# Optimization experiments

Measured on AMD Instinct MI355X. Metric: run time of the kernel, lower is better.

## Reference

```python
import jax, jax.numpy as jnp
import numpy as np

N = 1026; DX = 4096; DG = 4096; H0 = 4096; H1 = 2048; H2 = 1024
OUTS = 512; NL = 10; JH = 2048; E = 32832; K = 128; ALPHA = 0.05
INS = DX + DG  # 8192, edgeconv1 / joint_gemb input width

def _w(k, fan_in, shape):
    s = 1.0 / np.sqrt(fan_in)
    return jax.random.uniform(k, shape, minval=-s, maxval=s, dtype=jnp.float32)

def setup_inputs() -> dict:
    key = jax.random.key(0)
    ks = jax.random.split(key, 32)
    return dict(
        x=jax.random.normal(ks[0], (N, DX), jnp.float32),
        gx=jax.random.normal(ks[1], (N, DG), jnp.float32),
        edge_index=jax.random.randint(ks[2], (2, E), 0, N, dtype=jnp.int32),
        jw1=_w(ks[3], INS, (INS, JH)), jb1=_w(ks[4], INS, (JH,)),
        jw2=_w(ks[5], JH, (JH, N)), jb2=_w(ks[6], JH, (N,)),
        ec1_w=_w(ks[7], INS, (INS, H0)), ec1_b=_w(ks[8], INS, (H0,)),
        dr_w=_w(ks[9], H0, (H0, H2)), dr_b=_w(ks[10], H0, (H2,)),
        g1_w=_w(ks[11], H0, (H0, H1)), g1_b=_w(ks[12], H0, (H1,)),
        g2_w=_w(ks[13], H1, (H1, H2)), g2_b=_w(ks[14], H1, (H2,)),
        ec2_w=_w(ks[15], H2 + H1 + H0, (H2 + H1 + H0, H2)), ec2_b=_w(ks[16], H2 + H1 + H0, (H2,)),
        ec3_w=_w(ks[17], H2, (H2, OUTS)), ec3_b=_w(ks[18], H2, (OUTS,)),
        out_w=_w(ks[19], OUTS, (OUTS, NL)), out_b=_w(ks[20], OUTS, (NL,)),
    )

def _gdc(A):
    # GDC: self_loop_weight=1, sym norm in, exact PPR (alpha), topk(k, dim=0) sparsify, col norm out
    n = A.shape[0]
    eye = jnp.eye(n, dtype=A.dtype)
    A = A + eye  # self loops, weight 1
    deg = A.sum(axis=1)
    dinv = jax.lax.rsqrt(jnp.where(deg > 0, deg, 1.0))
    T = dinv[:, None] * A * dinv[None, :]          # D^-1/2 (A+I) D^-1/2
    S = ALPHA * jnp.linalg.inv(eye - (1.0 - ALPHA) * T)  # exact PPR diffusion
    vals, idx = jax.lax.top_k(S.T, K)              # top-K per column (dim=0)
    St = jnp.zeros((n, n), S.dtype).at[jnp.arange(n)[:, None], idx].set(vals)
    S = St.T
    csum = S.sum(axis=0)
    return S / jnp.where(csum == 0, 1.0, csum)[None, :]  # col normalization out

def _gcn(h_in, W, b, row, col, n):
    # PyG GCNConv: add self loops, sym-normalized aggregation, then bias
    h = h_in @ W
    deg = jax.ops.segment_sum(jnp.ones(row.shape[0], h.dtype), col, num_segments=n) + 1.0
    dinv = jax.lax.rsqrt(deg)
    agg = jax.ops.segment_sum(h[row] * (dinv[row] * dinv[col])[:, None], col, num_segments=n)
    return agg + h * (dinv * dinv)[:, None] + b

def _forward(x, gx, edge_index, jw1, jb1, jw2, jb2, ec1_w, ec1_b, dr_w, dr_b,
             g1_w, g1_b, g2_w, g2_b, ec2_w, ec2_b, ec3_w, ec3_b, out_w, out_b):
    row, col = edge_index[0], edge_index[1]
    xg = jnp.concatenate([x, gx], axis=1)                    # [N, INS]
    zz = jax.nn.relu(jax.nn.relu(xg @ jw1 + jb1) @ jw2 + jb2)  # joint_gemb -> [N, N] adjacency
    zz = _gdc(zz)
    xn = zz @ x                                              # nconv: dense neighbor aggregation
    z = jax.nn.relu(jnp.concatenate([xn, gx], axis=1) @ ec1_w + ec1_b)  # [N, H0]
    z0 = z @ dr_w + dr_b                                     # [N, H2]
    z1 = jax.nn.relu(_gcn(z + gx, g1_w, g1_b, row, col, N))  # [N, H1]
    z2 = jax.nn.relu(_gcn(z1, g2_w, g2_b, row, col, N))      # [N, H2]
    zc = jax.nn.relu(jnp.concatenate([z, z1, z2], axis=1) @ ec2_w + ec2_b)
    zf = jax.nn.relu((zc + z0) @ ec3_w + ec3_b)
    return zf @ out_w + out_b                                # [N, NL]

def reference(x, gx, edge_index, jw1, jb1, jw2, jb2, ec1_w, ec1_b, dr_w, dr_b,
              g1_w, g1_b, g2_w, g2_b, ec2_w, ec2_b, ec3_w, ec3_b, out_w, out_b):
    return _forward(x, gx, edge_index, jw1, jb1, jw2, jb2, ec1_w, ec1_b, dr_w, dr_b,
                    g1_w, g1_b, g2_w, g2_b, ec2_w, ec2_b, ec3_w, ec3_b, out_w, out_b)
```

## Files before the change

### kernel.cpp

```cpp
#include <hip/hip_runtime.h>
#include <stdint.h>

static constexpr int N_   = 1026;
static constexpr int DX_  = 4096;
static constexpr int DG_  = 4096;
static constexpr int H0_  = 4096;
static constexpr int H1_  = 2048;
static constexpr int H2_  = 1024;
static constexpr int OUTS_= 512;
static constexpr int NL_  = 10;
static constexpr int JH_  = 2048;
static constexpr int E_   = 32832;
static constexpr int K_   = 128;
static constexpr int INS_ = DX_ + DG_;
static constexpr int CAT2_= H0_ + H1_ + H2_;

static constexpr int MP_   = 1152;
static constexpr int KP1_  = 1056;

typedef _Float16 f16;
typedef __attribute__((ext_vector_type(8))) _Float16 f16x8;
typedef __attribute__((ext_vector_type(4))) _Float16 f16x4;
typedef __attribute__((ext_vector_type(4))) float    f32x4;

#define AS1C(p) ((const __attribute__((address_space(1))) unsigned int*)(p))
#define AS3(p)  ((__attribute__((address_space(3))) unsigned int*)(p))

__device__ __forceinline__ void gload16(const f16* g, f16* s) {
    __builtin_amdgcn_global_load_lds(AS1C(g), AS3(s), 16, 0, 0);
}

__device__ __forceinline__ void swz_tile(int gx, int gy, int& bx, int& by) {
    int nwg = gx * gy;
    int hid = blockIdx.x + gx * blockIdx.y;
    int xcd = hid & 7, seq = hid >> 3;
    int q = nwg >> 3, r = nwg & 7;
    int lin = (xcd < r ? xcd * (q + 1) : r * (q + 1) + (xcd - r) * q) + seq;
    bx = lin / gy;  by = lin - bx * gy;
}

template<bool RELU, bool DUAL, bool WIDE>
__global__ __launch_bounds__(512, (DUAL || WIDE) ? 4 : 8)
void gemm_f16x2(int M, int Nc, int Kt, int chunkSteps,
                const f16* __restrict__ Ah, const f16* __restrict__ Al, int lda,
                const f16* __restrict__ Bh, const f16* __restrict__ Bl, int ldb,
                const float* __restrict__ bias, float alpha,
                const float* __restrict__ D, int ldd, float dscale,
                float* __restrict__ C, int ldc,
                f16* __restrict__ oAh, f16* __restrict__ oAl, int ldoa,
                f16* __restrict__ oBh, f16* __restrict__ oBl, int ldob,
                float* __restrict__ P, int Mp, int Ncp)
// ... 157 lines not shown
        if (oAl) oAl[(size_t)row * ldoa + col] = (f16)(val - (float)h);
    }
    if (oBh) {
        f16 h = (f16)val;
        oBh[(size_t)col * ldob + row] = h;
        if (oBl) oBl[(size_t)col * ldob + row] = (f16)(val - (float)h);
    }
}

__global__ __launch_bounds__(512, 4)
void pchain_k(int roleBase, int split, int chunkSteps,
              const f16* __restrict__ uAh, const f16* __restrict__ uAl,
              const f16* __restrict__ sAh, const f16* __restrict__ sAl,
              const f16* __restrict__ Bh, const f16* __restrict__ Bl,
              float* __restrict__ Pp)
{
    __shared__ __align__(16) f16 sm[2][4][4096];
    const int tid  = threadIdx.x;
    const int lane = tid & 63, w = tid >> 6;
    const int wr = w >> 1, wc = w & 1;
    int bx, by; swz_tile(gridDim.x, gridDim.y, bx, by);
    const int bm = by * 128, bn = bx * 128;
    const int z = blockIdx.z;
    const int role = roleBase + z / split;
    const int sub  = z % split;
    const f16* Ah = (role == 0) ? uAh : sAh;
    const f16* Al = (role == 0) ? uAl : sAl;

    const int sBeg = sub * chunkSteps;
    int nst = KP1_ / 32 - sBeg; if (nst > chunkSteps) nst = chunkSteps;

    const int srow  = w * 16 + (tid & 15);
    const int skoff = ((tid >> 4) & 3) * 8;
    const size_t arow = (size_t)(bm + srow) * KP1_ + skoff;
    const size_t brow = (size_t)(bn + srow) * KP1_ + skoff;
    const int wslot = w * 512;
    const int fr = (lane >> 4) * 128 + (lane & 15) * 8;
    const int iaBase = wr * 1024 + fr;
    const int ibBase = wc * 2048 + fr;

    f32x4 acc[2][4] = {};

    auto stage = [&](int buf, size_t ka) {
        f16* s0 = (f16*)&sm[buf][0][0];
        gload16(Ah + arow + ka, s0 + wslot);
        gload16(Al + arow + ka, s0 + 4096 + wslot);
        gload16(Bh + brow + ka, s0 + 8192 + wslot);
        gload16(Bl + brow + ka, s0 + 12288 + wslot);
    };

    if (nst > 0) {
        const size_t kb = (size_t)sBeg * 32;
        stage(0, kb);
        for (int s = 0; s < nst; ++s) {
            if (s + 1 < nst) {
                stage((s + 1) & 1, kb + (size_t)(s + 1) * 32);
                asm volatile("s_waitcnt vmcnt(4)\n\ts_barrier" ::: "memory");
            } else {
                asm volatile("s_waitcnt vmcnt(0)\n\ts_barrier" ::: "memory");
            }
            const int b = s & 1;
            f16x8 ah[2], al[2], bh4[4], bl4[4];
            #pragma unroll
            for (int i = 0; i < 2; ++i) {
                ah[i]  = *(const f16x8*)&sm[b][0][iaBase + i * 512];
                al[i]  = *(const f16x8*)&sm[b][1][iaBase + i * 512];
            }
            #pragma unroll
// ... 21 lines not shown
    for (int mi = 0; mi < 2; ++mi)
        #pragma unroll
        for (int nj = 0; nj < 4; ++nj) {
            const int gc = n00 + nj * 16 + ec;
            const int gr = m00 + mi * 16 + er;
            float* p = Pz + (size_t)gr * 1152 + gc;
            f32x4 a = acc[mi][nj];
            #pragma unroll
            for (int r = 0; r < 4; ++r) p[(size_t)r * 1152] = a[r];
        }
}

__global__ __launch_bounds__(256)
void pchain_combine_k(int nz, int hasUpd, int hasSq, const float* __restrict__ Pp,
                      const float* __restrict__ PfIn, float* __restrict__ PfOut,
                      f16* __restrict__ oPh, f16* __restrict__ oPl,
                      float* __restrict__ XT,
                      f16* __restrict__ oAh, f16* __restrict__ oAl,
                      f16* __restrict__ oAth, f16* __restrict__ oAtl)
{
    unsigned idx = blockIdx.x * 256 + threadIdx.x;
    if (idx >= (unsigned)(N_ * N_)) return;
    int row = idx / (unsigned)N_, col = idx - row * N_;
    const size_t zs = (size_t)1152 * 1152;
    const size_t poff = (size_t)row * 1152 + col;
    int zb = 0;
    if (hasUpd) {
        float s = 0.f;
        for (int z = 0; z < nz; ++z) s += Pp[(size_t)(zb + z) * zs + poff];
        float val = s + PfIn[idx];
        PfOut[idx] = val;
        if (oPh) {
            f16 h = (f16)val, l = (f16)(val - (float)h);
            oPh[(size_t)row * KP1_ + col] = h;
            oPl[(size_t)row * KP1_ + col] = l;
        }
        if (XT) XT[(size_t)col * N_ + row] = val;
        zb += nz;
    }
    if (hasSq) {
        float s = 0.f;
        for (int z = 0; z < nz; ++z) s += Pp[(size_t)(zb + z) * zs + poff];
        f16 h = (f16)s, l = (f16)(s - (float)h);
        oAh[(size_t)row * KP1_ + col] = h;  oAl[(size_t)row * KP1_ + col] = l;
        oAth[(size_t)col * KP1_ + row] = h; oAtl[(size_t)col * KP1_ + row] = l;
    }
}

__global__ void build_A_k(const float* __restrict__ zz, const float* __restrict__ dinv,
                          f16* __restrict__ aAh, f16* __restrict__ aAl,
                          f16* __restrict__ aBth, f16* __restrict__ aBtl,
                          float* __restrict__ Pf,
                          f16* __restrict__ pAh, f16* __restrict__ pAl)
{
    int idx = blockIdx.x * 256 + threadIdx.x;
    if (idx >= N_ * N_) return;
    int i = idx / N_, j = idx - i * N_;
    float diag = (i == j) ? 1.f : 0.f;
    float a = 0.95f * dinv[i] * (zz[idx] + diag) * dinv[j];
    f16 h = (f16)a, l = (f16)(a - (float)h);
    aAh[(size_t)i * KP1_ + j] = h;  aAl[(size_t)i * KP1_ + j] = l;
    aBth[(size_t)j * KP1_ + i] = h; aBtl[(size_t)j * KP1_ + i] = l;
    float p = a + diag;
    Pf[idx] = p;
    f16 ph = (f16)p, pl = (f16)(p - (float)ph);
    pAh[(size_t)i * KP1_ + j] = ph; pAl[(size_t)i * KP1_ + j] = pl;
}

__global__ __launch_bounds__(256)
void topk_sort_k(const float* __restrict__ XT, float* __restrict__ S)
{
    __shared__ uint64_t key[2048];
    __shared__ float red[4];
    const int j = blockIdx.x, t = threadIdx.x;
    for (int i = t; i < 2048; i += 256) {
        uint64_t kk;
        if (i < N_) {
            float v = XT[(size_t)j * N_ + i];
            unsigned u = __float_as_uint(v);
            unsigned sv = (u & 0x80000000u) ? ~u : (u | 0x80000000u);
            kk = ((uint64_t)(~sv) << 32) | (unsigned)i;
        } else kk = ~0ULL;
        key[i] = kk;
    }
    __syncthreads();
    for (int k = 2; k <= 2048; k <<= 1) {
        for (int jj = k >> 1; jj > 0; jj >>= 1) {
            #pragma unroll
            for (int q = 0; q < 8; ++q) {
                int i = t + q * 256;
                int ixj = i ^ jj;
                if (ixj > i) {
                    uint64_t a = key[i], b = key[ixj];
                    bool up = ((i & k) == 0);
                    if ((a > b) == up) { key[i] = b; key[ixj] = a; }
                }
            }
            __syncthreads();
        }
    }
    float val = 0.f; int idx = 0;
    if (t < K_) {
        uint64_t kk = key[t];
        unsigned sv = ~(unsigned)(kk >> 32);
        unsigned u = (sv & 0x80000000u) ? (sv & 0x7FFFFFFFu) : ~sv;
        val = __uint_as_float(u);
        idx = (int)(kk & 0xFFFFFFFFu);
    }
    float sm = (t < K_) ? val : 0.f;
    #pragma unroll
    for (int q = 32; q > 0; q >>= 1) sm += __shfl_xor(sm, q);
    if ((t & 63) == 0) red[t >> 6] = sm;
    __syncthreads();
    float cs = red[0] + red[1] + red[2] + red[3];
    if (cs == 0.f) cs = 1.f;
    if (t < K_) S[(size_t)idx * N_ + j] = val / cs;
}

__global__ void conv_A_k(const float* __restrict__ src, int R, int C, int lds,
                         f16* __restrict__ dh, f16* __restrict__ dl, int ldd,
                         int Rp, int Cp)
{
    size_t i4 = ((size_t)blockIdx.x * 256 + threadIdx.x) * 4;
    if (i4 >= (size_t)Rp * Cp) return;
    int r = (int)(i4 / Cp), c = (int)(i4 % Cp);
    float v[4] = {0.f, 0.f, 0.f, 0.f};
    if (r < R) {
        if (((lds & 3) == 0) && c + 3 < C) {
            float4 f = *(const float4*)&src[(size_t)r * lds + c];
            v[0] = f.x; v[1] = f.y; v[2] = f.z; v[3] = f.w;
        } else {
            #pragma unroll
            for (int q = 0; q < 4; ++q) v[q] = (c + q < C) ? src[(size_t)r * lds + c + q] : 0.f;
        }
    }
    f16x4 h, l;
    #pragma unroll
    for (int q = 0; q < 4; ++q) { h[q] = (f16)v[q]; l[q] = (f16)(v[q] - (float)h[q]); }
    *(f16x4*)&dh[(size_t)r * ldd + c] = h;
    if (dl) *(f16x4*)&dl[(size_t)r * ldd + c] = l;
}

__global__ __launch_bounds__(256)
void conv_Bt_k(const float* __restrict__ src, int K, int N,
               f16* __restrict__ dh, f16* __restrict__ dl, int ldk,
               int Kp, int Np)
{
// ... 28 lines not shown
        #pragma unroll
        for (int p = 0; p < 2; ++p) {
            int n = bn + nn0 + p * 32;
            int k = bk + k4;
            if (n < Np && k < Kp) {
                f16x4 h, l;
                #pragma unroll
                for (int q = 0; q < 4; ++q) {
                    float vv = t[k4 + q][nn0 + p * 32];
                    h[q] = (f16)vv; l[q] = (f16)(vv - (float)h[q]);
                }
                *(f16x4*)&dh[(size_t)n * ldk + k] = h;
                if (dl) *(f16x4*)&dl[(size_t)n * ldk + k] = l;
            }
        }
    }
}

__global__ void cat2_conv_k(const float* __restrict__ a, const float* __restrict__ b,
                            f16* __restrict__ dh, f16* __restrict__ dl)
{
    size_t i4 = ((size_t)blockIdx.x * 256 + threadIdx.x) * 4;
    if (i4 >= (size_t)MP_ * 8192) return;
    int r = (int)(i4 / 8192), c = (int)(i4 % 8192);
    float v[4] = {0.f, 0.f, 0.f, 0.f};
    if (r < N_) {
        const float* s = (c < 4096) ? &a[(size_t)r * 4096 + c] : &b[(size_t)r * 4096 + (c - 4096)];
        float4 f = *(const float4*)s;
        v[0] = f.x; v[1] = f.y; v[2] = f.z; v[3] = f.w;
    }
    f16x4 h, l;
    #pragma unroll
    for (int q = 0; q < 4; ++q) { h[q] = (f16)v[q]; l[q] = (f16)(v[q] - (float)h[q]); }
    *(f16x4*)&dh[i4] = h;
    *(f16x4*)&dl[i4] = l;
}

__global__ void zgx_conv_k(const f16* __restrict__ zh, const float* __restrict__ gx,
                           f16* __restrict__ dh)
{
    size_t i4 = ((size_t)blockIdx.x * 256 + threadIdx.x) * 4;
    if (i4 >= (size_t)MP_ * 4096) return;
    int r = (int)(i4 / 4096), c = (int)(i4 % 4096);
    f16x4 h = {};
    if (r < N_) {
        f16x4 zh4 = *(const f16x4*)&zh[(size_t)r * CAT2_ + c];
        float4 g4 = *(const float4*)&gx[(size_t)r * 4096 + c];
        float gv[4] = {g4.x, g4.y, g4.z, g4.w};
        #pragma unroll
        for (int q = 0; q < 4; ++q) h[q] = (f16)((float)zh4[q] + gv[q]);
    }
    *(f16x4*)&dh[i4] = h;
}

__global__ void zc_conv_k(const float* __restrict__ zc, const float* __restrict__ z0,
                          f16* __restrict__ dh)
{
    size_t i4 = ((size_t)blockIdx.x * 256 + threadIdx.x) * 4;
    if (i4 >= (size_t)MP_ * 1024) return;
    int r = (int)(i4 / 1024), c = (int)(i4 % 1024);
    f16x4 h = {};
    if (r < N_) {
        float4 a4 = *(const float4*)&zc[(size_t)r * 1024 + c];
        float4 b4 = *(const float4*)&z0[(size_t)r * 1024 + c];
        float av[4] = {a4.x, a4.y, a4.z, a4.w};
        float bv[4] = {b4.x, b4.y, b4.z, b4.w};
        #pragma unroll
        for (int q = 0; q < 4; ++q) h[q] = (f16)(av[q] + bv[q]);
    }
    *(f16x4*)&dh[i4] = h;
}

template<int NPARTS, bool RELU>
__global__ __launch_bounds__(256)
void gemm_k(int M, int Nc, int Kt,
            const float* __restrict__ A0, int w0,
            const float* __restrict__ A1, int w1,
            const float* __restrict__ A2, int w2,
            const float* __restrict__ B, int ldb,
            const float* __restrict__ bias,
            float alpha, const float* __restrict__ D, float dscale,
            float* __restrict__ C, int ldc)
{
    __shared__ __align__(16) float As[16][68];
    __shared__ __align__(16) float Bs[16][68];
    const int tid = threadIdx.x;
    const int tx = tid & 15, ty = tid >> 4;
    const int bm = blockIdx.y * 64, bn = blockIdx.x * 64;
    const int w01 = w0 + w1;
    float acc[4][4] = {};

    for (int kt = 0; kt < Kt; kt += 16) {
        #pragma unroll
        for (int r = 0; r < 4; ++r) {
            int idx = tid + r * 256;
            int m = idx >> 4, kk = idx & 15;
            int row = bm + m, k = kt + kk;
            float v = 0.f;
            if (row < M && k < Kt) {
                if (NPARTS == 1) v = A0[(size_t)row * w0 + k];
                else {
                    if (k < w0) v = A0[(size_t)row * w0 + k];
                    else if (NPARTS == 2 || k < w01) v = A1[(size_t)row * w1 + (k - w0)];
// ... 194 lines not shown
            combine_k<false><<<cg, 256, 0, st>>>(M, Nc, split, Mp, Ncp, P, bias, alpha,
                D, ldd, dscale, C, ldc, oA.h, oA.l, ldoa, oB.h, oB.l, ldob);
    }
}

static inline void convA(hipStream_t st, const float* src, int R, int C, int lds,
                         HL d, int ldd, int Rp, int Cp)
{
    size_t total4 = (size_t)Rp * Cp / 4;
    conv_A_k<<<(int)((total4 + 255) / 256), 256, 0, st>>>(src, R, C, lds, d.h, d.l, ldd, Rp, Cp);
}
static inline void convBt(hipStream_t st, const float* src, int K, int N,
                          HL d, int ldk, int Kp, int Np)
{
    dim3 grid((Kp + 31) / 32, (Np + 63) / 64), blk(256);
    conv_Bt_k<<<grid, blk, 0, st>>>(src, K, N, d.h, d.l, ldk, Kp, Np);
}

static inline void launch_gemm_f32(hipStream_t st, bool relu, int nparts,
                                   int M, int Nc, int Kt,
                                   const float* A0, int w0, const float* A1, int w1,
                                   const float* A2, int w2,
                                   const float* B, int ldb, const float* bias,
                                   float alpha, const float* D, float dscale,
                                   float* C, int ldc)
{
    dim3 g((Nc + 63) / 64, (M + 63) / 64), b(256);
#define CALL_GEMM(NP, RL) gemm_k<NP, RL><<<g, b, 0, st>>>(M, Nc, Kt, A0, w0, A1, w1, A2, w2, B, ldb, bias, alpha, D, dscale, C, ldc)
    if (relu) { if (nparts == 1) CALL_GEMM(1, true); else if (nparts == 2) CALL_GEMM(2, true); else CALL_GEMM(3, true); }
    else      { if (nparts == 1) CALL_GEMM(1, false); else if (nparts == 2) CALL_GEMM(2, false); else CALL_GEMM(3, false); }
#undef CALL_GEMM
}

static constexpr size_t catA1_e = (size_t)MP_ * 8192;
static constexpr size_t jw1Bt_e = (size_t)2048 * 8192;
static constexpr size_t jw2Bt_e = (size_t)MP_ * 2048;
static constexpr size_t h1A_e   = (size_t)MP_ * 2048;
static constexpr size_t nb_e    = (size_t)MP_ * KP1_;
static constexpr size_t ec1Bt_e = (size_t)4096 * 8192;
static constexpr size_t drBt_e  = (size_t)1024 * 4096;
static constexpr size_t g1Bt_e  = (size_t)2048 * 4096;
static constexpr size_t g2Bt_e  = (size_t)1024 * 2048;
static constexpr size_t ec2Bt_e = (size_t)1024 * 7168;
static constexpr size_t ec3Bt_e = (size_t)512 * 1024;
static constexpr size_t hg1Bt_e = (size_t)2048 * KP1_;
static constexpr size_t hg2Bt_e = (size_t)1024 * KP1_;
static constexpr size_t catA2_e = (size_t)MP_ * 8192;
static constexpr size_t SA_e    = nb_e;
static constexpr size_t GA_e    = nb_e;
static constexpr size_t xBt_e   = (size_t)4096 * KP1_;
static constexpr size_t zgxA_e  = (size_t)MP_ * 4096;
static constexpr size_t cat3_e  = (size_t)MP_ * 7168;
static constexpr size_t zcA_e   = (size_t)MP_ * 1024;

static constexpr size_t u_catA1 = 0;
static constexpr size_t u_jw1Bt = u_catA1 + 2 * catA1_e;
static constexpr size_t u_jw2Bt = u_jw1Bt + 2 * jw1Bt_e;
static constexpr size_t u_h1A   = u_jw2Bt + 2 * jw2Bt_e;
static constexpr size_t u_nb0   = u_h1A + 2 * h1A_e;
static constexpr size_t u_nb1   = u_nb0 + 2 * nb_e;
static constexpr size_t u_nb2   = u_nb1 + 2 * nb_e;
static constexpr size_t u_nb3   = u_nb2 + 2 * nb_e;
static constexpr size_t u_nb4   = u_nb3 + 2 * nb_e;
static constexpr size_t u_nb5   = u_nb4 + 2 * nb_e;
static constexpr size_t UNION_F16 = u_nb5 + 2 * nb_e;
static_assert(2 * ec1Bt_e <= UNION_F16, "ec1Bt alias");
static constexpr size_t u_drBt  = 0;
static constexpr size_t u_g1Bt  = u_drBt + 2 * drBt_e;
static constexpr size_t u_g2Bt  = u_g1Bt + 2 * g1Bt_e;
static constexpr size_t u_ec2Bt = u_g2Bt + 2 * g2Bt_e;
static constexpr size_t u_ec3Bt = u_ec2Bt + 2 * ec2Bt_e;
static constexpr size_t u_hg1Bt = u_ec3Bt + 2 * ec3Bt_e;
static constexpr size_t u_hg2Bt = u_hg1Bt + 2 * hg1Bt_e;
static_assert(u_hg2Bt + 2 * hg2Bt_e <= UNION_F16, "phase3 alias");

static constexpr size_t o_catA2 = 0;
static constexpr size_t o_SA    = o_catA2 + 2 * catA2_e;
static constexpr size_t o_GA    = o_SA + 2 * SA_e;
static constexpr size_t o_xBt   = o_GA + 2 * GA_e;
static constexpr size_t o_zgxA  = o_xBt + 2 * xBt_e;
static constexpr size_t o_cat3  = o_zgxA + 2 * zgxA_e;
static constexpr size_t o_zcA   = o_cat3 + 2 * cat3_e;
static constexpr size_t OUT_F16 = o_zcA + 2 * zcA_e;

static constexpr size_t NN_     = (size_t)N_ * N_;
static constexpr size_t F16_TOTAL = UNION_F16 + OUT_F16;
static constexpr size_t f_zz = 0, f_Mm = NN_, f_X0 = 2 * NN_, f_X1 = 3 * NN_,
                        f_S = 4 * NN_, f_G = 5 * NN_, f_z0 = 6 * NN_,
                        f_zc = f_z0 + (size_t)N_ * 1024,
                        f_zf = f_zc + (size_t)N_ * 1024,
                        f_dinv = f_zf + (size_t)N_ * 512,
                        f_dinv2 = f_dinv + 1028,
                        F32_TOTAL = f_dinv2 + 1028;
static constexpr size_t P_e = (size_t)2 * MP_ * 4096;
static constexpr size_t FAST_WS_BYTES = F16_TOTAL * 2 + (F32_TOTAL + P_e) * 4;
static_assert((size_t)6 * 1152 * 1152 <= P_e, "pchain partial fit");
static_assert((size_t)8 * 1152 * 1024 <= P_e, "wide split8 fit");
static_assert((size_t)4 * 1152 * 2048 <= P_e, "wide split4 fit");

static void run_fast(void* const* d_in, float* out, void* d_ws, hipStream_t st)
{
    const float* x    = (const float*)d_in[0];
    const float* gx   = (const float*)d_in[1];
    const int*   ei   = (const int*)d_in[2];
    const float* jw1  = (const float*)d_in[3];
    const float* jb1  = (const float*)d_in[4];
    const float* jw2  = (const float*)d_in[5];
    const float* jb2  = (const float*)d_in[6];
    const float* ec1w = (const float*)d_in[7];
    const float* ec1b = (const float*)d_in[8];
    const float* drw  = (const float*)d_in[9];
    const float* drb  = (const float*)d_in[10];
    const float* g1w  = (const float*)d_in[11];
    const float* g1b  = (const float*)d_in[12];
    const float* g2w  = (const float*)d_in[13];
    const float* g2b  = (const float*)d_in[14];
    const float* ec2w = (const float*)d_in[15];
    const float* ec2b = (const float*)d_in[16];
    const float* ec3w = (const float*)d_in[17];
    const float* ec3b = (const float*)d_in[18];
    const float* outw = (const float*)d_in[19];
    const float* outb = (const float*)d_in[20];

    f16*   fb   = (f16*)d_ws;
    float* f32b = (float*)((char*)d_ws + F16_TOTAL * 2);
    float* P    = f32b + F32_TOTAL;

    auto mk = [&](size_t off, size_t elems) { return HL{fb + off, fb + off + elems}; };
    HL catA1 = mk(u_catA1, catA1_e), jw1Bt = mk(u_jw1Bt, jw1Bt_e),
       jw2Bt = mk(u_jw2Bt, jw2Bt_e), h1A = mk(u_h1A, h1A_e);
    HL pA[2]  = {mk(u_nb0, nb_e), mk(u_nb1, nb_e)};
    HL aA[2]  = {mk(u_nb2, nb_e), mk(u_nb3, nb_e)};
    HL aBt[2] = {mk(u_nb4, nb_e), mk(u_nb5, nb_e)};
    HL ec1Bt = mk(0, ec1Bt_e);
    HL drBt = mk(u_drBt, drBt_e), g1Bt = mk(u_g1Bt, g1Bt_e), g2Bt = mk(u_g2Bt, g2Bt_e),
       ec2Bt = mk(u_ec2Bt, ec2Bt_e), ec3Bt = mk(u_ec3Bt, ec3Bt_e),
       hg1Bt = mk(u_hg1Bt, hg1Bt_e), hg2Bt = mk(u_hg2Bt, hg2Bt_e);
    HL catA2 = mk(UNION_F16 + o_catA2, catA2_e), SA = mk(UNION_F16 + o_SA, SA_e),
       GA = mk(UNION_F16 + o_GA, GA_e), xBt = mk(UNION_F16 + o_xBt, xBt_e),
       zgxA = mk(UNION_F16 + o_zgxA, zgxA_e), cat3 = mk(UNION_F16 + o_cat3, cat3_e),
       zcA = mk(UNION_F16 + o_zcA, zcA_e);
    float *zz = f32b + f_zz, *XT = f32b + f_Mm, *Pf[2] = {f32b + f_X0, f32b + f_X1},
          *S = f32b + f_S, *G = f32b + f_G, *z0 = f32b + f_z0, *zc = f32b + f_zc,
          *zf = f32b + f_zf, *dinv = f32b + f_dinv, *dinv2 = f32b + f_dinv2;

    hipMemsetAsync(fb + u_nb0, 0, (UNION_F16 - u_nb0) * sizeof(f16), st);

    {
        size_t t4 = (size_t)MP_ * 8192 / 4;
        cat2_conv_k<<<(int)((t4 + 255) / 256), 256, 0, st>>>(x, gx, catA1.h, catA1.l);
    }
    convBt(st, jw1, 8192, 2048, jw1Bt, 8192, 8192, 2048);
    g16(st, true, true, false, 1026, 2048, 8192, 4, catA1, 8192, jw1Bt, 8192, jb1, 1.f,
        nullptr, 0, 0.f, nullptr, 0, h1A, 2048, HL0, 0, P);
    convBt(st, jw2, 2048, 1026, jw2Bt, 2048, 2048, MP_);
    g16(st, true, true, false, 1026, 1026, 2048, 7, h1A, 2048, jw2Bt, 2048, jb2, 1.f,
        nullptr, 0, 0.f, zz, 1026, HL0, 0, HL0, 0, P);
    row_dinv_k<<<N_, 256, 0, st>>>(zz, dinv);
    build_A_k<<<(int)((NN_ + 255) / 256), 256, 0, st>>>(zz, dinv,
        aA[0].h, aA[0].l, aBt[0].h, aBt[0].l, Pf[0], pA[0].h, pA[0].l);
    {
        const int PS = 3, PCH = 11;
        dim3 cg((unsigned)((NN_ + 255) / 256));
        pchain_k<<<dim3(9, 9, PS), 512, 0, st>>>(1, PS, PCH,
            nullptr, nullptr, aA[0].h, aA[0].l, aBt[0].h, aBt[0].l, P);
        pchain_combine_k<<<cg, 256, 0, st>>>(PS, 0, 1, P,
            nullptr, nullptr, nullptr, nullptr, nullptr,
            aA[1].h, aA[1].l, aBt[1].h, aBt[1].l);
        int ac = 1, pc = 0;
        for (int k = 2; k <= 7; ++k) {
            pchain_k<<<dim3(9, 9, 2 * PS), 512, 0, st>>>(0, PS, PCH,
                pA[pc].h, pA[pc].l, aA[ac].h, aA[ac].l, aBt[ac].h, aBt[ac].l, P);
            pchain_combine_k<<<cg, 256, 0, st>>>(PS, 1, 1, P,
                Pf[pc], Pf[1 - pc], pA[1 - pc].h, pA[1 - pc].l, nullptr,
                aA[1 - ac].h, aA[1 - ac].l, aBt[1 - ac].h, aBt[1 - ac].l);
            pc ^= 1; ac ^= 1;
        }
        pchain_k<<<dim3(9, 9, PS), 512, 0, st>>>(0, PS, PCH,
            pA[pc].h, pA[pc].l, nullptr, nullptr, aBt[ac].h, aBt[ac].l, P);
        pchain_combine_k<<<cg, 256, 0, st>>>(PS, 1, 0, P,
            Pf[pc], Pf[1 - pc], nullptr, nullptr, XT,
            nullptr, nullptr, nullptr, nullptr);
    }
    hipMemsetAsync(S, 0, NN_ * sizeof(float), st);
    topk_sort_k<<<N_, 256, 0, st>>>(XT, S);
    convA(st, S, N_, N_, N_, SA, KP1_, MP_, KP1_);
    convBt(st, x, 1026, 4096, xBt, KP1_, KP1_, 4096);
    g16(st, false, true, false, 1026, 4096, KP1_, 2, SA, KP1_, xBt, KP1_, nullptr, 1.f,
        nullptr, 0, 0.f, nullptr, 0, HL{catA2.h, nullptr}, 8192, HL0, 0, P);
    convA(st, gx, N_, 4096, 4096, HL{catA2.h + 4096, nullptr}, 8192, MP_, 4096);
    convBt(st, ec1w, 8192, 4096, HL{ec1Bt.h, nullptr}, 8192, 8192, 4096);
    g16(st, true, false, true, 1026, 4096, 8192, 2, catA2, 8192, ec1Bt, 8192, ec1b, 1.f,
        nullptr, 0, 0.f, nullptr, 0, HL{cat3.h, nullptr}, 7168, HL0, 0, P);
    deg_dinv_k<<<1, 1024, 0, st>>>(ei, dinv2);
    hipMemsetAsync(G, 0, NN_ * sizeof(float), st);
    edge_diag_G_k<<<(E_ + N_ + 255) / 256, 256, 0, st>>>(ei, dinv2, G);
    convA(st, G, N_, N_, N_, HL{GA.h, nullptr}, KP1_, MP_, KP1_);
    convBt(st, drw, 4096, 1024, HL{drBt.h, nullptr}, 4096, 4096, 1024);
    g16(st, false, false, true, 1026, 1024, 4096, 8, HL{cat3.h, nullptr}, 7168,
        drBt, 4096, drb, 1.f, nullptr, 0, 0.f, z0, 1024, HL0, 0, HL0, 0, P);
    {
        size_t t4 = (size_t)MP_ * 4096 / 4;
        zgx_conv_k<<<(int)((t4 + 255) / 256), 256, 0, st>>>(cat3.h, gx, zgxA.h);
    }
    convBt(st, g1w, 4096, 2048, HL{g1Bt.h, nullptr}, 4096, 4096, 2048);
    hipMemsetAsync(fb + u_hg1Bt, 0, (2 * hg1Bt_e + 2 * hg2Bt_e) * sizeof(f16), st);
    g16(st, false, false, false, 2048, 1026, 4096, 4, g1Bt, 4096, zgxA, 4096, nullptr, 1.f,
        nullptr, 0, 0.f, nullptr, 0, HL{hg1Bt.h, nullptr}, KP1_, HL0, 0, P);
    g16(st, true, false, true, 1026, 2048, KP1_, 4, GA, KP1_, hg1Bt, KP1_, g1b, 1.f,
        nullptr, 0, 0.f, nullptr, 0, HL{cat3.h + 4096, nullptr}, 7168, HL0, 0, P);
    convBt(st, g2w, 2048, 1024, HL{g2Bt.h, nullptr}, 2048, 2048, 1024);
    g16(st, false, false, false, 1024, 1026, 2048, 8, g2Bt, 2048,
        HL{cat3.h + 4096, nullptr}, 7168, nullptr, 1.f, nullptr, 0, 0.f,
        nullptr, 0, HL{hg2Bt.h, nullptr}, KP1_, HL0, 0, P);
    g16(st, true, false, true, 1026, 1024, KP1_, 8, GA, KP1_, hg2Bt, KP1_, g2b, 1.f,
        nullptr, 0, 0.f, nullptr, 0, HL{cat3.h + 6144, nullptr}, 7168, HL0, 0, P);
    convBt(st, ec2w, 7168, 1024, HL{ec2Bt.h, nullptr}, 7168, 7168, 1024);
    g16(st, true, false, true, 1026, 1024, 7168, 8, HL{cat3.h, nullptr}, 7168,
        ec2Bt, 7168, ec2b, 1.f, nullptr, 0, 0.f, zc, 1024, HL0, 0, HL0, 0, P);
    {
        size_t t4 = (size_t)MP_ * 1024 / 4;
        zc_conv_k<<<(int)((t4 + 255) / 256), 256, 0, st>>>(zc, z0, zcA.h);
    }
    convBt(st, ec3w, 1024, 512, HL{ec3Bt.h, nullptr}, 1024, 1024, 512);
    g16(st, true, false, false, 1026, 512, 1024, 8, HL{zcA.h, nullptr}, 1024,
        ec3Bt, 1024, ec3b, 1.f, nullptr, 0, 0.f, zf, 512, HL0, 0, HL0, 0, P);
    launch_gemm_f32(st, false, 1, N_, NL_, OUTS_, zf, OUTS_, nullptr, 0, nullptr, 0,
                    outw, NL_, outb, 1.f, nullptr, 0.f, out, NL_);
}

static void run_ref(void* const* d_in, float* out, void* d_ws, hipStream_t stream)
{
    const float* x    = (const float*)d_in[0];
    const float* gx   = (const float*)d_in[1];
    const int*   ei   = (const int*)d_in[2];
    const float* jw1  = (const float*)d_in[3];
    const float* jb1  = (const float*)d_in[4];
    const float* jw2  = (const float*)d_in[5];
    const float* jb2  = (const float*)d_in[6];
    const float* ec1w = (const float*)d_in[7];
    const float* ec1b = (const float*)d_in[8];
    const float* drw  = (const float*)d_in[9];
    const float* drb  = (const float*)d_in[10];
    const float* g1w  = (const float*)d_in[11];
    const float* g1b  = (const float*)d_in[12];
    const float* g2w  = (const float*)d_in[13];
    const float* g2b  = (const float*)d_in[14];
    const float* ec2w = (const float*)d_in[15];
    const float* ec2b = (const float*)d_in[16];
    const float* ec3w = (const float*)d_in[17];
    const float* ec3b = (const float*)d_in[18];
    const float* outw = (const float*)d_in[19];
    const float* outb = (const float*)d_in[20];

    float* ws = (float*)d_ws;
    size_t off = 0;
    float* H1buf = ws + off; off += (size_t)N_ * JH_;
    float* ZZ    = ws + off; off += NN_;
    float* Mm    = ws + off; off += NN_;
// ... 74 lines not shown
```

Measured before the change: 1.478 ms.

## Pad f16 operand leading dimensions by 64 and widen top-k sort blocks

Adds 64 elements of padding to the leading dimension of every f16 GEMM operand buffer (INS, JH, H0, CAT3, H2, NB). The likely aim is to stop power-of-two row strides from landing repeatedly on the same memory channels or cache sets. Buffers that only ever hold a high part now get single-sized allocations, which shrinks the workspace. The top-k bitonic sort now runs with 512 threads per block instead of 256, halving the per-thread work in each phase. All call sites and conversion kernels are updated, so a missed stride would silently corrupt results.

```diff
diff --git a/kernel.cpp b/kernel.cpp
--- a/kernel.cpp
+++ b/kernel.cpp
@@ -17,6 +17,13 @@
 
 static constexpr int MP_   = 1152;
 static constexpr int KP1_  = 1056;
+
+static constexpr int LD_INS  = INS_ + 64;
+static constexpr int LD_JH   = JH_  + 64;
+static constexpr int LD_H0   = H0_  + 64;
+static constexpr int LD_CAT3 = CAT2_+ 64;
+static constexpr int LD_H2   = H2_  + 64;
+static constexpr int LD_NB   = KP1_ + 64;
 
 typedef _Float16 f16;
 typedef __attribute__((ext_vector_type(8))) _Float16 f16x8;
@@ -240,8 +247,8 @@
 
     const int srow  = w * 16 + (tid & 15);
     const int skoff = ((tid >> 4) & 3) * 8;
-    const size_t arow = (size_t)(bm + srow) * KP1_ + skoff;
-    const size_t brow = (size_t)(bn + srow) * KP1_ + skoff;
+    const size_t arow = (size_t)(bm + srow) * LD_NB + skoff;
+    const size_t brow = (size_t)(bn + srow) * LD_NB + skoff;
     const int wslot = w * 512;
     const int fr = (lane >> 4) * 128 + (lane & 15) * 8;
     const int iaBase = wr * 1024 + fr;
@@ -329,8 +336,8 @@
         PfOut[idx] = val;
         if (oPh) {
             f16 h = (f16)val, l = (f16)(val - (float)h);
-            oPh[(size_t)row * KP1_ + col] = h;
-            oPl[(size_t)row * KP1_ + col] = l;
+            oPh[(size_t)row * LD_NB + col] = h;
+            oPl[(size_t)row * LD_NB + col] = l;
         }
         if (XT) XT[(size_t)col * N_ + row] = val;
         zb += nz;
@@ -339,8 +346,8 @@
         float s = 0.f;
         for (int z = 0; z < nz; ++z) s += Pp[(size_t)(zb + z) * zs + poff];
         f16 h = (f16)s, l = (f16)(s - (float)h);
-        oAh[(size_t)row * KP1_ + col] = h;  oAl[(size_t)row * KP1_ + col] = l;
-        oAth[(size_t)col * KP1_ + row] = h; oAtl[(size_t)col * KP1_ + row] = l;
+        oAh[(size_t)row * LD_NB + col] = h;  oAl[(size_t)row * LD_NB + col] = l;
+        oAth[(size_t)col * LD_NB + row] = h; oAtl[(size_t)col * LD_NB + row] = l;
     }
 }
 
@@ -356,21 +363,21 @@
     float diag = (i == j) ? 1.f : 0.f;
     float a = 0.95f * dinv[i] * (zz[idx] + diag) * dinv[j];
     f16 h = (f16)a, l = (f16)(a - (float)h);
-    aAh[(size_t)i * KP1_ + j] = h;  aAl[(size_t)i * KP1_ + j] = l;
-    aBth[(size_t)j * KP1_ + i] = h; aBtl[(size_t)j * KP1_ + i] = l;
+    aAh[(size_t)i * LD_NB + j] = h;  aAl[(size_t)i * LD_NB + j] = l;
+    aBth[(size_t)j * LD_NB + i] = h; aBtl[(size_t)j * LD_NB + i] = l;
     float p = a + diag;
     Pf[idx] = p;
     f16 ph = (f16)p, pl = (f16)(p - (float)ph);
-    pAh[(size_t)i * KP1_ + j] = ph; pAl[(size_t)i * KP1_ + j] = pl;
-}
-
-__global__ __launch_bounds__(256)
+    pAh[(size_t)i * LD_NB + j] = ph; pAl[(size_t)i * LD_NB + j] = pl;
+}
+
+__global__ __launch_bounds__(512)
 void topk_sort_k(const float* __restrict__ XT, float* __restrict__ S)
 {
     __shared__ uint64_t key[2048];
-    __shared__ float red[4];
+    __shared__ float red[8];
     const int j = blockIdx.x, t = threadIdx.x;
-    for (int i = t; i < 2048; i += 256) {
+    for (int i = t; i < 2048; i += 512) {
         uint64_t kk;
         if (i < N_) {
             float v = XT[(size_t)j * N_ + i];
@@ -384,8 +391,8 @@
     for (int k = 2; k <= 2048; k <<= 1) {
         for (int jj = k >> 1; jj > 0; jj >>= 1) {
             #pragma unroll
-            for (int q = 0; q < 8; ++q) {
-                int i = t + q * 256;
+            for (int q = 0; q < 4; ++q) {
+                int i = t + q * 512;
                 int ixj = i ^ jj;
                 if (ixj > i) {
                     uint64_t a = key[i], b = key[ixj];
@@ -409,7 +416,9 @@
     for (int q = 32; q > 0; q >>= 1) sm += __shfl_xor(sm, q);
     if ((t & 63) == 0) red[t >> 6] = sm;
     __syncthreads();
-    float cs = red[0] + red[1] + red[2] + red[3];
+    float cs = 0.f;
+    #pragma unroll
+    for (int q = 0; q < 8; ++q) cs += red[q];
     if (cs == 0.f) cs = 1.f;
     if (t < K_) S[(size_t)idx * N_ + j] = val / cs;
 }
@@ -504,8 +513,8 @@
     f16x4 h, l;
     #pragma unroll
     for (int q = 0; q < 4; ++q) { h[q] = (f16)v[q]; l[q] = (f16)(v[q] - (float)h[q]); }
-    *(f16x4*)&dh[i4] = h;
-    *(f16x4*)&dl[i4] = l;
+    *(f16x4*)&dh[(size_t)r * LD_INS + c] = h;
+    *(f16x4*)&dl[(size_t)r * LD_INS + c] = l;
 }
 
 __global__ void zgx_conv_k(const f16* __restrict__ zh, const float* __restrict__ gx,
@@ -516,13 +525,13 @@
     int r = (int)(i4 / 4096), c = (int)(i4 % 4096);
     f16x4 h = {};
     if (r < N_) {
-        f16x4 zh4 = *(const f16x4*)&zh[(size_t)r * CAT2_ + c];
+        f16x4 zh4 = *(const f16x4*)&zh[(size_t)r * LD_CAT3 + c];
         float4 g4 = *(const float4*)&gx[(size_t)r * 4096 + c];
         float gv[4] = {g4.x, g4.y, g4.z, g4.w};
         #pragma unroll
         for (int q = 0; q < 4; ++q) h[q] = (f16)((float)zh4[q] + gv[q]);
     }
-    *(f16x4*)&dh[i4] = h;
+    *(f16x4*)&dh[(size_t)r * LD_H0 + c] = h;
 }
 
 __global__ void zc_conv_k(const float* __restrict__ zc, const float* __restrict__ z0,
@@ -540,7 +549,7 @@
         #pragma unroll
         for (int q = 0; q < 4; ++q) h[q] = (f16)(av[q] + bv[q]);
     }
-    *(f16x4*)&dh[i4] = h;
+    *(f16x4*)&dh[(size_t)r * LD_H2 + c] = h;
 }
 
 template<int NPARTS, bool RELU>
@@ -801,26 +810,26 @@
 #undef CALL_GEMM
 }
 
-static constexpr size_t catA1_e = (size_t)MP_ * 8192;
-static constexpr size_t jw1Bt_e = (size_t)2048 * 8192;
-static constexpr size_t jw2Bt_e = (size_t)MP_ * 2048;
-static constexpr size_t h1A_e   = (size_t)MP_ * 2048;
-static constexpr size_t nb_e    = (size_t)MP_ * KP1_;
-static constexpr size_t ec1Bt_e = (size_t)4096 * 8192;
-static constexpr size_t drBt_e  = (size_t)1024 * 4096;
-static constexpr size_t g1Bt_e  = (size_t)2048 * 4096;
-static constexpr size_t g2Bt_e  = (size_t)1024 * 2048;
-static constexpr size_t ec2Bt_e = (size_t)1024 * 7168;
-static constexpr size_t ec3Bt_e = (size_t)512 * 1024;
-static constexpr size_t hg1Bt_e = (size_t)2048 * KP1_;
-static constexpr size_t hg2Bt_e = (size_t)1024 * KP1_;
-static constexpr size_t catA2_e = (size_t)MP_ * 8192;
+static constexpr size_t catA1_e = (size_t)MP_ * LD_INS;
+static constexpr size_t jw1Bt_e = (size_t)2048 * LD_INS;
+static constexpr size_t jw2Bt_e = (size_t)MP_ * LD_JH;
+static constexpr size_t h1A_e   = (size_t)MP_ * LD_JH;
+static constexpr size_t nb_e    = (size_t)MP_ * LD_NB;
+static constexpr size_t ec1Bt_e = (size_t)4096 * LD_INS;
+static constexpr size_t drBt_e  = (size_t)1024 * LD_H0;
+static constexpr size_t g1Bt_e  = (size_t)2048 * LD_H0;
+static constexpr size_t g2Bt_e  = (size_t)1024 * LD_JH;
+static constexpr size_t ec2Bt_e = (size_t)1024 * LD_CAT3;
+static constexpr size_t ec3Bt_e = (size_t)512 * LD_H2;
+static constexpr size_t hg1Bt_e = (size_t)2048 * LD_NB;
+static constexpr size_t hg2Bt_e = (size_t)1024 * LD_NB;
+static constexpr size_t catA2_e = (size_t)MP_ * LD_INS;
 static constexpr size_t SA_e    = nb_e;
 static constexpr size_t GA_e    = nb_e;
-static constexpr size_t xBt_e   = (size_t)4096 * KP1_;
-static constexpr size_t zgxA_e  = (size_t)MP_ * 4096;
-static constexpr size_t cat3_e  = (size_t)MP_ * 7168;
-static constexpr size_t zcA_e   = (size_t)MP_ * 1024;
+static constexpr size_t xBt_e   = (size_t)4096 * LD_NB;
+static constexpr size_t zgxA_e  = (size_t)MP_ * LD_H0;
+static constexpr size_t cat3_e  = (size_t)MP_ * LD_CAT3;
+static constexpr size_t zcA_e   = (size_t)MP_ * LD_H2;
 
 static constexpr size_t u_catA1 = 0;
 static constexpr size_t u_jw1Bt = u_catA1 + 2 * catA1_e;
@@ -833,24 +842,24 @@
 static constexpr size_t u_nb4   = u_nb3 + 2 * nb_e;
 static constexpr size_t u_nb5   = u_nb4 + 2 * nb_e;
 static constexpr size_t UNION_F16 = u_nb5 + 2 * nb_e;
-static_assert(2 * ec1Bt_e <= UNION_F16, "ec1Bt alias");
+static_assert(ec1Bt_e <= UNION_F16, "ec1Bt alias");
 static constexpr size_t u_drBt  = 0;
-static constexpr size_t u_g1Bt  = u_drBt + 2 * drBt_e;
-static constexpr size_t u_g2Bt  = u_g1Bt + 2 * g1Bt_e;
-static constexpr size_t u_ec2Bt = u_g2Bt + 2 * g2Bt_e;
-static constexpr size_t u_ec3Bt = u_ec2Bt + 2 * ec2Bt_e;
-static constexpr size_t u_hg1Bt = u_ec3Bt + 2 * ec3Bt_e;
-static constexpr size_t u_hg2Bt = u_hg1Bt + 2 * hg1Bt_e;
-static_assert(u_hg2Bt + 2 * hg2Bt_e <= UNION_F16, "phase3 alias");
+static constexpr size_t u_g1Bt  = u_drBt + drBt_e;
+static constexpr size_t u_g2Bt  = u_g1Bt + g1Bt_e;
+static constexpr size_t u_ec2Bt = u_g2Bt + g2Bt_e;
+static constexpr size_t u_ec3Bt = u_ec2Bt + ec2Bt_e;
+static constexpr size_t u_hg1Bt = u_ec3Bt + ec3Bt_e;
+static constexpr size_t u_hg2Bt = u_hg1Bt + hg1Bt_e;
+static_assert(u_hg2Bt + hg2Bt_e <= UNION_F16, "phase3 alias");
 
 static constexpr size_t o_catA2 = 0;
-static constexpr size_t o_SA    = o_catA2 + 2 * catA2_e;
+static constexpr size_t o_SA    = o_catA2 + catA2_e;
 static constexpr size_t o_GA    = o_SA + 2 * SA_e;
-static constexpr size_t o_xBt   = o_GA + 2 * GA_e;
+static constexpr size_t o_xBt   = o_GA + GA_e;
 static constexpr size_t o_zgxA  = o_xBt + 2 * xBt_e;
-static constexpr size_t o_cat3  = o_zgxA + 2 * zgxA_e;
-static constexpr size_t o_zcA   = o_cat3 + 2 * cat3_e;
-static constexpr size_t OUT_F16 = o_zcA + 2 * zcA_e;
+static constexpr size_t o_cat3  = o_zgxA + zgxA_e;
+static constexpr size_t o_zcA   = o_cat3 + cat3_e;
+static constexpr size_t OUT_F16 = o_zcA + zcA_e;
 
 static constexpr size_t NN_     = (size_t)N_ * N_;
 static constexpr size_t F16_TOTAL = UNION_F16 + OUT_F16;
@@ -895,20 +904,21 @@
     float* f32b = (float*)((char*)d_ws + F16_TOTAL * 2);
     float* P    = f32b + F32_TOTAL;
 
-    auto mk = [&](size_t off, size_t elems) { return HL{fb + off, fb + off + elems}; };
-    HL catA1 = mk(u_catA1, catA1_e), jw1Bt = mk(u_jw1Bt, jw1Bt_e),
-       jw2Bt = mk(u_jw2Bt, jw2Bt_e), h1A = mk(u_h1A, h1A_e);
-    HL pA[2]  = {mk(u_nb0, nb_e), mk(u_nb1, nb_e)};
-    HL aA[2]  = {mk(u_nb2, nb_e), mk(u_nb3, nb_e)};
-    HL aBt[2] = {mk(u_nb4, nb_e), mk(u_nb5, nb_e)};
-    HL ec1Bt = mk(0, ec1Bt_e);
-    HL drBt = mk(u_drBt, drBt_e), g1Bt = mk(u_g1Bt, g1Bt_e), g2Bt = mk(u_g2Bt, g2Bt_e),
-       ec2Bt = mk(u_ec2Bt, ec2Bt_e), ec3Bt = mk(u_ec3Bt, ec3Bt_e),
-       hg1Bt = mk(u_hg1Bt, hg1Bt_e), hg2Bt = mk(u_hg2Bt, hg2Bt_e);
-    HL catA2 = mk(UNION_F16 + o_catA2, catA2_e), SA = mk(UNION_F16 + o_SA, SA_e),
-       GA = mk(UNION_F16 + o_GA, GA_e), xBt = mk(UNION_F16 + o_xBt, xBt_e),
-       zgxA = mk(UNION_F16 + o_zgxA, zgxA_e), cat3 = mk(UNION_F16 + o_cat3, cat3_e),
-       zcA = mk(UNION_F16 + o_zcA, zcA_e);
+    auto mk2 = [&](size_t off, size_t elems) { return HL{fb + off, fb + off + elems}; };
+    auto mk1 = [&](size_t off) { return HL{fb + off, nullptr}; };
+    HL catA1 = mk2(u_catA1, catA1_e), jw1Bt = mk2(u_jw1Bt, jw1Bt_e),
+       jw2Bt = mk2(u_jw2Bt, jw2Bt_e), h1A = mk2(u_h1A, h1A_e);
+    HL pA[2]  = {mk2(u_nb0, nb_e), mk2(u_nb1, nb_e)};
+    HL aA[2]  = {mk2(u_nb2, nb_e), mk2(u_nb3, nb_e)};
+    HL aBt[2] = {mk2(u_nb4, nb_e), mk2(u_nb5, nb_e)};
+    HL ec1Bt = mk1(0);
+    HL drBt = mk1(u_drBt), g1Bt = mk1(u_g1Bt), g2Bt = mk1(u_g2Bt),
+       ec2Bt = mk1(u_ec2Bt), ec3Bt = mk1(u_ec3Bt),
+       hg1Bt = mk1(u_hg1Bt), hg2Bt = mk1(u_hg2Bt);
+    HL catA2 = mk1(UNION_F16 + o_catA2), SA = mk2(UNION_F16 + o_SA, SA_e),
+       GA = mk1(UNION_F16 + o_GA), xBt = mk2(UNION_F16 + o_xBt, xBt_e),
+       zgxA = mk1(UNION_F16 + o_zgxA), cat3 = mk1(UNION_F16 + o_cat3),
+       zcA = mk1(UNION_F16 + o_zcA);
     float *zz = f32b + f_zz, *XT = f32b + f_Mm, *Pf[2] = {f32b + f_X0, f32b + f_X1},
           *S = f32b + f_S, *G = f32b + f_G, *z0 = f32b + f_z0, *zc = f32b + f_zc,
           *zf = f32b + f_zf, *dinv = f32b + f_dinv, *dinv2 = f32b + f_dinv2;
@@ -919,11 +929,11 @@
         size_t t4 = (size_t)MP_ * 8192 / 4;
         cat2_conv_k<<<(int)((t4 + 255) / 256), 256, 0, st>>>(x, gx, catA1.h, catA1.l);
     }
-    convBt(st, jw1, 8192, 2048, jw1Bt, 8192, 8192, 2048);
-    g16(st, true, true, false, 1026, 2048, 8192, 4, catA1, 8192, jw1Bt, 8192, jb1, 1.f,
-        nullptr, 0, 0.f, nullptr, 0, h1A, 2048, HL0, 0, P);
-    convBt(st, jw2, 2048, 1026, jw2Bt, 2048, 2048, MP_);
-    g16(st, true, true, false, 1026, 1026, 2048, 7, h1A, 2048, jw2Bt, 2048, jb2, 1.f,
+    convBt(st, jw1, 8192, 2048, jw1Bt, LD_INS, 8192, 2048);
+    g16(st, true, true, false, 1026, 2048, 8192, 4, catA1, LD_INS, jw1Bt, LD_INS, jb1, 1.f,
+        nullptr, 0, 0.f, nullptr, 0, h1A, LD_JH, HL0, 0, P);
+    convBt(st, jw2, 2048, 1026, jw2Bt, LD_JH, 2048, MP_);
+    g16(st, true, true, false, 1026, 1026, 2048, 7, h1A, LD_JH, jw2Bt, LD_JH, jb2, 1.f,
         nullptr, 0, 0.f, zz, 1026, HL0, 0, HL0, 0, P);
     row_dinv_k<<<N_, 256, 0, st>>>(zz, dinv);
     build_A_k<<<(int)((NN_ + 255) / 256), 256, 0, st>>>(zz, dinv,
@@ -952,48 +962,48 @@
             nullptr, nullptr, nullptr, nullptr);
     }
     hipMemsetAsync(S, 0, NN_ * sizeof(float), st);
-    topk_sort_k<<<N_, 256, 0, st>>>(XT, S);
-    convA(st, S, N_, N_, N_, SA, KP1_, MP_, KP1_);
-    convBt(st, x, 1026, 4096, xBt, KP1_, KP1_, 4096);
-    g16(st, false, true, false, 1026, 4096, KP1_, 2, SA, KP1_, xBt, KP1_, nullptr, 1.f,
-        nullptr, 0, 0.f, nullptr, 0, HL{catA2.h, nullptr}, 8192, HL0, 0, P);
-    convA(st, gx, N_, 4096, 4096, HL{catA2.h + 4096, nullptr}, 8192, MP_, 4096);
-    convBt(st, ec1w, 8192, 4096, HL{ec1Bt.h, nullptr}, 8192, 8192, 4096);
-    g16(st, true, false, true, 1026, 4096, 8192, 2, catA2, 8192, ec1Bt, 8192, ec1b, 1.f,
-        nullptr, 0, 0.f, nullptr, 0, HL{cat3.h, nullptr}, 7168, HL0, 0, P);
+    topk_sort_k<<<N_, 512, 0, st>>>(XT, S);
+    convA(st, S, N_, N_, N_, SA, LD_NB, MP_, KP1_);
+    convBt(st, x, 1026, 4096, xBt, LD_NB, KP1_, 4096);
+    g16(st, false, true, false, 1026, 4096, KP1_, 2, SA, LD_NB, xBt, LD_NB, nullptr, 1.f,
+        nullptr, 0, 0.f, nullptr, 0, HL{catA2.h, nullptr}, LD_INS, HL0, 0, P);
+    convA(st, gx, N_, 4096, 4096, HL{catA2.h + 4096, nullptr}, LD_INS, MP_, 4096);
+    convBt(st, ec1w, 8192, 4096, ec1Bt, LD_INS, 8192, 4096);
+    g16(st, true, false, true, 1026, 4096, 8192, 2, catA2, LD_INS, ec1Bt, LD_INS, ec1b, 1.f,
+        nullptr, 0, 0.f, nullptr, 0, HL{cat3.h, nullptr}, LD_CAT3, HL0, 0, P);
     deg_dinv_k<<<1, 1024, 0, st>>>(ei, dinv2);
     hipMemsetAsync(G, 0, NN_ * sizeof(float), st);
     edge_diag_G_k<<<(E_ + N_ + 255) / 256, 256, 0, st>>>(ei, dinv2, G);
-    convA(st, G, N_, N_, N_, HL{GA.h, nullptr}, KP1_, MP_, KP1_);
-    convBt(st, drw, 4096, 1024, HL{drBt.h, nullptr}, 4096, 4096, 1024);
-    g16(st, false, false, true, 1026, 1024, 4096, 8, HL{cat3.h, nullptr}, 7168,
-        drBt, 4096, drb, 1.f, nullptr, 0, 0.f, z0, 1024, HL0, 0, HL0, 0, P);
+    convA(st, G, N_, N_, N_, GA, LD_NB, MP_, KP1_);
+    convBt(st, drw, 4096, 1024, drBt, LD_H0, 4096, 1024);
+    g16(st, false, false, true, 1026, 1024, 4096, 8, HL{cat3.h, nullptr}, LD_CAT3,
+        drBt, LD_H0, drb, 1.f, nullptr, 0, 0.f, z0, 1024, HL0, 0, HL0, 0, P);
     {
         size_t t4 = (size_t)MP_ * 4096 / 4;
         zgx_conv_k<<<(int)((t4 + 255) / 256), 256, 0, st>>>(cat3.h, gx, zgxA.h);
     }
-    convBt(st, g1w, 4096, 2048, HL{g1Bt.h, nullptr}, 4096, 4096, 2048);
-    hipMemsetAsync(fb + u_hg1Bt, 0, (2 * hg1Bt_e + 2 * hg2Bt_e) * sizeof(f16), st);
-    g16(st, false, false, false, 2048, 1026, 4096, 4, g1Bt, 4096, zgxA, 4096, nullptr, 1.f,
-        nullptr, 0, 0.f, nullptr, 0, HL{hg1Bt.h, nullptr}, KP1_, HL0, 0, P);
-    g16(st, true, false, true, 1026, 2048, KP1_, 4, GA, KP1_, hg1Bt, KP1_, g1b, 1.f,
-        nullptr, 0, 0.f, nullptr, 0, HL{cat3.h + 4096, nullptr}, 7168, HL0, 0, P);
-    convBt(st, g2w, 2048, 1024, HL{g2Bt.h, nullptr}, 2048, 2048, 1024);
-    g16(st, false, false, false, 1024, 1026, 2048, 8, g2Bt, 2048,
-        HL{cat3.h + 4096, nullptr}, 7168, nullptr, 1.f, nullptr, 0, 0.f,
-        nullptr, 0, HL{hg2Bt.h, nullptr}, KP1_, HL0, 0, P);
-    g16(st, true, false, true, 1026, 1024, KP1_, 8, GA, KP1_, hg2Bt, KP1_, g2b, 1.f,
-        nullptr, 0, 0.f, nullptr, 0, HL{cat3.h + 6144, nullptr}, 7168, HL0, 0, P);
-    convBt(st, ec2w, 7168, 1024, HL{ec2Bt.h, nullptr}, 7168, 7168, 1024);
-    g16(st, true, false, true, 1026, 1024, 7168, 8, HL{cat3.h, nullptr}, 7168,
-        ec2Bt, 7168, ec2b, 1.f, nullptr, 0, 0.f, zc, 1024, HL0, 0, HL0, 0, P);
+    convBt(st, g1w, 4096, 2048, g1Bt, LD_H0, 4096, 2048);
+    hipMemsetAsync(fb + u_hg1Bt, 0, (hg1Bt_e + hg2Bt_e) * sizeof(f16), st);
+    g16(st, false, false, false, 2048, 1026, 4096, 4, g1Bt, LD_H0, zgxA, LD_H0, nullptr, 1.f,
+        nullptr, 0, 0.f, nullptr, 0, HL{hg1Bt.h, nullptr}, LD_NB, HL0, 0, P);
+    g16(st, true, false, true, 1026, 2048, KP1_, 4, GA, LD_NB, hg1Bt, LD_NB, g1b, 1.f,
+        nullptr, 0, 0.f, nullptr, 0, HL{cat3.h + 4096, nullptr}, LD_CAT3, HL0, 0, P);
+    convBt(st, g2w, 2048, 1024, g2Bt, LD_JH, 2048, 1024);
+    g16(st, false, false, false, 1024, 1026, 2048, 8, g2Bt, LD_JH,
+        HL{cat3.h + 4096, nullptr}, LD_CAT3, nullptr, 1.f, nullptr, 0, 0.f,
+        nullptr, 0, HL{hg2Bt.h, nullptr}, LD_NB, HL0, 0, P);
+    g16(st, true, false, true, 1026, 1024, KP1_, 8, GA, LD_NB, hg2Bt, LD_NB, g2b, 1.f,
+        nullptr, 0, 0.f, nullptr, 0, HL{cat3.h + 6144, nullptr}, LD_CAT3, HL0, 0, P);
+    convBt(st, ec2w, 7168, 1024, ec2Bt, LD_CAT3, 7168, 1024);
+    g16(st, true, false, true, 1026, 1024, 7168, 8, HL{cat3.h, nullptr}, LD_CAT3,
+        ec2Bt, LD_CAT3, ec2b, 1.f, nullptr, 0, 0.f, zc, 1024, HL0, 0, HL0, 0, P);
     {
         size_t t4 = (size_t)MP_ * 1024 / 4;
         zc_conv_k<<<(int)((t4 + 255) / 256), 256, 0, st>>>(zc, z0, zcA.h);
     }
-    convBt(st, ec3w, 1024, 512, HL{ec3Bt.h, nullptr}, 1024, 1024, 512);
-    g16(st, true, false, false, 1026, 512, 1024, 8, HL{zcA.h, nullptr}, 1024,
-        ec3Bt, 1024, ec3b, 1.f, nullptr, 0, 0.f, zf, 512, HL0, 0, HL0, 0, P);
+    convBt(st, ec3w, 1024, 512, ec3Bt, LD_H2, 1024, 512);
+    g16(st, true, false, false, 1026, 512, 1024, 8, HL{zcA.h, nullptr}, LD_H2,
+        ec3Bt, LD_H2, ec3b, 1.f, nullptr, 0, 0.f, zf, 512, HL0, 0, HL0, 0, P);
     launch_gemm_f32(st, false, 1, N_, NL_, OUTS_, zf, OUTS_, nullptr, 0, nullptr, 0,
                     outw, NL_, outb, 1.f, nullptr, 0.f, out, NL_);
 }
```

Result: no change. 1.500 ms (+1.5%).
